# Performance work log

Measured on AMD Instinct MI355X. Metric: run time of the kernel, lower is better.

Reference implementation:

```python
import jax, jax.numpy as jnp
import numpy as np

N, E, IN_DIM, HID, LAYERS = 300000, 600000, 64, 128, 2
BN_EPS = 1e-5

def setup_inputs() -> dict:
    key = jax.random.key(0)
    ks = jax.random.split(key, 8)
    scale_in = 1.0 / np.sqrt(IN_DIM)
    scale_h = 1.0 / np.sqrt(HID)
    return {
        "node_init": jax.random.normal(ks[0], (N, IN_DIM), dtype=jnp.float32),
        "edge_index": jax.random.randint(ks[1], (2, E), 0, N, dtype=jnp.int64),
        "edge_len": jax.random.uniform(ks[2], (E,), dtype=jnp.float32),
        "W_in": jax.random.normal(ks[3], (IN_DIM, HID), dtype=jnp.float32) * scale_in,
        "b_in": jnp.zeros((HID,), dtype=jnp.float32),
        "att_k": jax.random.normal(ks[4], (HID,), dtype=jnp.float32),
        "Wl": jax.random.normal(ks[5], (LAYERS, HID, HID), dtype=jnp.float32) * scale_h,
        "bl": jnp.zeros((LAYERS, HID), dtype=jnp.float32),
        "gamma": jnp.ones((LAYERS, HID), dtype=jnp.float32),
        "beta": jnp.zeros((LAYERS, HID), dtype=jnp.float32),
    }

def reference(node_init, edge_index, edge_len, W_in, b_in, att_k, Wl, bl, gamma, beta):
    src, dst = edge_index[0], edge_index[1]
    inv_len = 1.0 / (1.0 + edge_len)                     # [E]
    inv_sqrt_h = 1.0 / jnp.sqrt(jnp.asarray(HID, node_init.dtype))
    h = node_init @ W_in + b_in                          # [N,H]
    n = h.shape[0]
    for l in range(LAYERS):
        h_src = h[src]                                   # [E,H] gather
        key = (h_src @ att_k) * inv_sqrt_h               # [E]
        w = jnp.exp(key) * inv_len                       # [E]
        agg = jax.ops.segment_sum(w[:, None] * h_src, dst, num_segments=n)  # [N,H]
        h = h + jax.nn.relu(agg) @ Wl[l] + bl[l]
        mean = jnp.mean(h, axis=0)
        var = jnp.mean((h - mean) ** 2, axis=0)          # biased var (BatchNorm training)
        h = (h - mean) * jax.lax.rsqrt(var + BN_EPS) * gamma[l] + beta[l]
    return h
```

## Files before the change

kernel.cpp:

```cpp
#include <hip/hip_runtime.h>
#include <hip/hip_bf16.h>

#define N_NODES 300000
#define N_EDGES 600000
#define IN_DIMC 64
#define HIDC    128
#define NLAYERS 2
#define BN_EPS  1e-5f
#define INV_SQRT_H 0.08838834764831845f
#define NB_SCAN ((N_NODES + 255) / 256)
#define NTILES  (N_NODES / 16)

typedef __bf16 bf16x8 __attribute__((ext_vector_type(8)));
typedef float floatx4 __attribute__((ext_vector_type(4)));

__device__ int   g_row_ptr[N_NODES + 1];
__device__ int   g_cursor[N_NODES];
__device__ __align__(8) int2 g_edge[N_EDGES];
__device__ __align__(8) int2 g_ew[N_EDGES];
__device__ int   g_bsum[NB_SCAN];
__device__ float g_ekey[N_NODES];
__device__ __align__(16) __hip_bfloat16 g_Win_hi[128 * 64];
__device__ __align__(16) __hip_bfloat16 g_Win_lo[128 * 64];
__device__ __align__(16) __hip_bfloat16 g_Wl_hi[NLAYERS * 128 * 128];
__device__ __align__(16) __hip_bfloat16 g_Wl_lo[NLAYERS * 128 * 128];
__device__ float g_stats[NLAYERS * 2 * HIDC];
__device__ __align__(16) float g_bn_sc[NLAYERS * HIDC];
__device__ __align__(16) float g_bn_sh[NLAYERS * HIDC];

__device__ inline void split2(float x, __hip_bfloat16& hi, __hip_bfloat16& lo) {
    hi = __float2bfloat16(x);
    lo = __float2bfloat16(x - __bfloat162float(hi));
}

__global__ void zero_kernel() {
    int i = blockIdx.x * 256 + threadIdx.x;
    if (i < N_NODES) g_cursor[i] = 0;
    if (i < NLAYERS * 2 * HIDC) g_stats[i] = 0.f;
}

__global__ void prep_w_kernel(const float* __restrict__ W_in,
                              const float* __restrict__ Wl)
{
    int id = blockIdx.x * 256 + threadIdx.x;
    if (id < 128 * 64) {
        int n = id >> 6, k = id & 63;
        split2(W_in[k * 128 + n], g_Win_hi[id], g_Win_lo[id]);
    }
    if (id < NLAYERS * 128 * 128) {
        int l = id >> 14, r = id & 16383;
        int n = r >> 7, k = r & 127;
        split2(Wl[l * 16384 + k * 128 + n], g_Wl_hi[id], g_Wl_lo[id]);
    }
}

__global__ void hist_kernel(const int* __restrict__ dst)
{
    int e = blockIdx.x * 256 + threadIdx.x;
    if (e < N_EDGES) atomicAdd(&g_cursor[dst[e]], 1);
}

__global__ void scan1_kernel()
{
    __shared__ int tmp[256];
    int t = threadIdx.x;
    int i = blockIdx.x * 256 + t;
    tmp[t] = (i < N_NODES) ? g_cursor[i] : 0;
    __syncthreads();
    for (int d = 128; d > 0; d >>= 1) {
        if (t < d) tmp[t] += tmp[t + d];
        __syncthreads();
    }
    if (t == 0) g_bsum[blockIdx.x] = tmp[0];
}

__global__ void scan2_kernel()
{
    __shared__ int tmp[256];
    __shared__ int carry;
    int t = threadIdx.x;
    if (t == 0) { carry = 0; g_row_ptr[N_NODES] = N_EDGES; }
    __syncthreads();
    for (int base = 0; base < NB_SCAN; base += 256) {
        int i = base + t;
        int v = (i < NB_SCAN) ? g_bsum[i] : 0;
        tmp[t] = v;
        __syncthreads();
        for (int d = 1; d < 256; d <<= 1) {
            int x = (t >= d) ? tmp[t - d] : 0;
            __syncthreads();
            tmp[t] += x;
            __syncthreads();
        }
        int c = carry;
        if (i < NB_SCAN) g_bsum[i] = c + tmp[t] - v;
        __syncthreads();
        if (t == 0) carry = c + tmp[255];
        __syncthreads();
    }
}

__global__ void scan3_kernel()
{
    __shared__ int tmp[256];
    int t = threadIdx.x;
    int i = blockIdx.x * 256 + t;
    int v = (i < N_NODES) ? g_cursor[i] : 0;
    tmp[t] = v;
    __syncthreads();
    for (int d = 1; d < 256; d <<= 1) {
        int x = (t >= d) ? tmp[t - d] : 0;
        __syncthreads();
        tmp[t] += x;
        __syncthreads();
    }
    int r = g_bsum[blockIdx.x] + tmp[t] - v;
    if (i < N_NODES) { g_row_ptr[i] = r; g_cursor[i] = r; }
}

__global__ void scatter_kernel(const int* __restrict__ src, const int* __restrict__ dst,
                               const float* __restrict__ elen)
{
    int e = blockIdx.x * 256 + threadIdx.x;
    if (e >= N_EDGES) return;
    int d = dst[e];
    int pos = atomicAdd(&g_cursor[d], 1);
    int2 ed;
    ed.x = src[e];
    ed.y = __float_as_int(1.0f / (1.0f + elen[e]));
    g_edge[pos] = ed;
}

__global__ __launch_bounds__(256) void wt_kernel()
{
    int e = blockIdx.x * 256 + threadIdx.x;
    if (e >= N_EDGES) return;
    int2 ed = g_edge[e];
    int2 ew;
    ew.x = ed.x;
    ew.y = __float_as_int(g_ekey[ed.x] * __int_as_float(ed.y));
    g_ew[e] = ew;
}

__global__ __launch_bounds__(256) void edge_csr_kernel(
    const float* __restrict__ h, __hip_bfloat16* __restrict__ agg_hi,
    __hip_bfloat16* __restrict__ agg_lo, int prev)
{
    int lane = threadIdx.x & 63;
    int n = blockIdx.x * 4 + (threadIdx.x >> 6);
    if (n >= N_NODES) return;
    int beg = g_row_ptr[n], end = g_row_ptr[n + 1];
    float a0 = 0.f, a1 = 0.f, sw = 0.f;
    const float2* h2 = (const float2*)h;
    for (int j = beg; j < end; j += 4) {
        int2 e0 = g_ew[j];
        int2 e1 = (j + 1 < end) ? g_ew[j + 1] : make_int2(e0.x, 0);
        int2 e2 = (j + 2 < end) ? g_ew[j + 2] : make_int2(e0.x, 0);
        int2 e3 = (j + 3 < end) ? g_ew[j + 3] : make_int2(e0.x, 0);
        float w0 = __int_as_float(e0.y);
        float w1 = __int_as_float(e1.y);
        float w2 = __int_as_float(e2.y);
        float w3 = __int_as_float(e3.y);
        float2 x0 = h2[(size_t)e0.x * 64 + lane];
        float2 x1 = h2[(size_t)e1.x * 64 + lane];
        float2 x2 = h2[(size_t)e2.x * 64 + lane];
        float2 x3 = h2[(size_t)e3.x * 64 + lane];
        a0 += w0 * x0.x + w1 * x1.x + w2 * x2.x + w3 * x3.x;
        a1 += w0 * x0.y + w1 * x1.y + w2 * x2.y + w3 * x3.y;
        sw += w0 + w1 + w2 + w3;
    }
    float2 sc = make_float2(1.f, 1.f), sh = make_float2(0.f, 0.f);
    if (prev >= 0) {
        sc = ((const float2*)(g_bn_sc + prev * HIDC))[lane];
        sh = ((const float2*)(g_bn_sh + prev * HIDC))[lane];
    }
    float o0 = fmaxf(sc.x * a0 + sh.x * sw, 0.f);
    float o1 = fmaxf(sc.y * a1 + sh.y * sw, 0.f);
    union { __hip_bfloat16 e[2]; unsigned u; } ph, pl;
    split2(o0, ph.e[0], pl.e[0]);
    split2(o1, ph.e[1], pl.e[1]);
    ((unsigned*)agg_hi)[(size_t)n * 64 + lane] = ph.u;
    ((unsigned*)agg_lo)[(size_t)n * 64 + lane] = pl.u;
}

__global__ __launch_bounds__(256) void proj_mfma_kernel(
    const float* __restrict__ X, const float* __restrict__ b,
    const float* __restrict__ att_k, float* __restrict__ h)
{
    __shared__ __align__(16) __hip_bfloat16 Ah[64 * 72];
    __shared__ __align__(16) __hip_bfloat16 Al[64 * 72];
    __shared__ __align__(16) __hip_bfloat16 Bh[128 * 72];
    __shared__ __align__(16) __hip_bfloat16 Bl[128 * 72];
    int t = threadIdx.x;
    int nbase = blockIdx.x * 64;

    for (int i = t; i < 1024; i += 256) {
        int row = i >> 3, c8 = i & 7;
        *(float4*)((char*)Bh + row * 144 + c8 * 16) =
            *(const float4*)((const char*)g_Win_hi + row * 128 + c8 * 16);
        *(float4*)((char*)Bl + row * 144 + c8 * 16) =
            *(const float4*)((const char*)g_Win_lo + row * 128 + c8 * 16);
    }
    for (int i = t; i < 1024; i += 256) {
        int row = i >> 4, c4 = i & 15;
        int n = nbase + row;
        float4 v = make_float4(0.f, 0.f, 0.f, 0.f);
        if (n < N_NODES) v = *(const float4*)(X + (size_t)n * IN_DIMC + c4 * 4);
        union { __hip_bfloat16 e[4]; uint2 u; } ph, pl;
        split2(v.x, ph.e[0], pl.e[0]); split2(v.y, ph.e[1], pl.e[1]);
        split2(v.z, ph.e[2], pl.e[2]); split2(v.w, ph.e[3], pl.e[3]);
        *(uint2*)((char*)Ah + row * 144 + c4 * 8) = ph.u;
        *(uint2*)((char*)Al + row * 144 + c4 * 8) = pl.u;
    }
    __syncthreads();

    int lane = t & 63, w = t >> 6;
    int m16 = lane & 15, quad = lane >> 4;
    floatx4 acc[8];
#pragma unroll
    for (int i = 0; i < 8; ++i) acc[i] = floatx4{0.f, 0.f, 0.f, 0.f};

#pragma unroll
    for (int kk = 0; kk < 64; kk += 32) {
        bf16x8 ah = *(const bf16x8*)((const char*)Ah + (w * 16 + m16) * 144 + (kk + quad * 8) * 2);
        bf16x8 al = *(const bf16x8*)((const char*)Al + (w * 16 + m16) * 144 + (kk + quad * 8) * 2);
#pragma unroll
        for (int nt = 0; nt < 8; ++nt) {
            bf16x8 bh = *(const bf16x8*)((const char*)Bh + (nt * 16 + m16) * 144 + (kk + quad * 8) * 2);
            bf16x8 bl = *(const bf16x8*)((const char*)Bl + (nt * 16 + m16) * 144 + (kk + quad * 8) * 2);
            acc[nt] = __builtin_amdgcn_mfma_f32_16x16x32_bf16(ah, bh, acc[nt], 0, 0, 0);
            acc[nt] = __builtin_amdgcn_mfma_f32_16x16x32_bf16(al, bh, acc[nt], 0, 0, 0);
            acc[nt] = __builtin_amdgcn_mfma_f32_16x16x32_bf16(ah, bl, acc[nt], 0, 0, 0);
        }
    }
    float dotr[4] = {0.f, 0.f, 0.f, 0.f};
#pragma unroll
    for (int nt = 0; nt < 8; ++nt) {
        int ch = nt * 16 + m16;
        float bias = b[ch];
        float ak = att_k[ch];
#pragma unroll
        for (int r = 0; r < 4; ++r) {
            int n = nbase + w * 16 + quad * 4 + r;
            float o = acc[nt][r] + bias;
            if (n < N_NODES) h[(size_t)n * HIDC + ch] = o;
            dotr[r] += ak * o;
        }
    }
#pragma unroll
    for (int r = 0; r < 4; ++r) {
        float p = dotr[r];
        p += __shfl_xor(p, 1); p += __shfl_xor(p, 2);
        p += __shfl_xor(p, 4); p += __shfl_xor(p, 8);
        int n = nbase + w * 16 + quad * 4 + r;
        if (m16 == 0 && n < N_NODES) g_ekey[n] = __expf(p * INV_SQRT_H);
    }
}

__global__ __launch_bounds__(256) void key_kernel(const float* __restrict__ h,
                                                  const float* __restrict__ att_k,
                                                  int prev)
{
    int t = threadIdx.x;
    int lane = t & 63;
    int half = lane >> 5, sub = lane & 31;
    int n = (blockIdx.x * 4 + (t >> 6)) * 2 + half;
    if (n >= N_NODES) return;
    float4 x = ((const float4*)h)[(size_t)n * 32 + sub];
    float4 sc = ((const float4*)(g_bn_sc + prev * HIDC))[sub];
    float4 sh = ((const float4*)(g_bn_sh + prev * HIDC))[sub];
    float4 ak = ((const float4*)att_k)[sub];
    float p = (sc.x * x.x + sh.x) * ak.x + (sc.y * x.y + sh.y) * ak.y +
              (sc.z * x.z + sh.z) * ak.z + (sc.w * x.w + sh.w) * ak.w;
    p += __shfl_xor(p, 1);  p += __shfl_xor(p, 2);
    p += __shfl_xor(p, 4);  p += __shfl_xor(p, 8);
    p += __shfl_xor(p, 16);
    if (sub == 0) g_ekey[n] = __expf(p * INV_SQRT_H);
}

__global__ __launch_bounds__(256) void layer_gemm_kernel(
    float* __restrict__ h, const __hip_bfloat16* __restrict__ agg_hi,
    const __hip_bfloat16* __restrict__ agg_lo,
    const float* __restrict__ b, int layer, int prev)
{
    __shared__ __align__(16) __hip_bfloat16 Bh[128 * 136];
    __shared__ __align__(16) __hip_bfloat16 Bl[128 * 136];
    __shared__ float red[256];
    int t = threadIdx.x;
    const __hip_bfloat16* Wh = g_Wl_hi + layer * 16384;
    const __hip_bfloat16* Wlo = g_Wl_lo + layer * 16384;
    red[t] = 0.f;

    for (int i = t; i < 2048; i += 256) {
        int row = i >> 4, c8 = i & 15;
        *(float4*)((char*)Bh + row * 272 + c8 * 16) =
            *(const float4*)((const char*)Wh + row * 256 + c8 * 16);
        *(float4*)((char*)Bl + row * 272 + c8 * 16) =
            *(const float4*)((const char*)Wlo + row * 256 + c8 * 16);
    }
    __syncthreads();

    const int lane = t & 63, w = t >> 6;
    const int m16 = lane & 15, quad = lane >> 4;
    const int wid = blockIdx.x * 4 + w;
    const int nwaves = gridDim.x * 4;

    float bias[8], scp[8], shp[8];
#pragma unroll
    for (int nt = 0; nt < 8; ++nt) {
        int ch = nt * 16 + m16;
        bias[nt] = b[ch];
        scp[nt] = (prev >= 0) ? g_bn_sc[prev * HIDC + ch] : 1.f;
        shp[nt] = (prev >= 0) ? g_bn_sh[prev * HIDC + ch] : 0.f;
    }
    float sreg[8], qreg[8];
#pragma unroll
    for (int nt = 0; nt < 8; ++nt) { sreg[nt] = 0.f; qreg[nt] = 0.f; }

    for (int tile = wid; tile < NTILES; tile += nwaves) {
        const __hip_bfloat16* ahp = agg_hi + (size_t)(tile * 16 + m16) * HIDC + quad * 8;
        const __hip_bfloat16* alp = agg_lo + (size_t)(tile * 16 + m16) * HIDC + quad * 8;
        floatx4 acc[8];
#pragma unroll
        for (int i = 0; i < 8; ++i) acc[i] = floatx4{0.f, 0.f, 0.f, 0.f};

#pragma unroll
        for (int kk = 0; kk < 4; ++kk) {
            bf16x8 ah = *(const bf16x8*)(ahp + kk * 32);
            bf16x8 al = *(const bf16x8*)(alp + kk * 32);
#pragma unroll
            for (int nt = 0; nt < 8; ++nt) {
                bf16x8 bh = *(const bf16x8*)((const char*)Bh + (nt * 16 + m16) * 272 + (kk * 32 + quad * 8) * 2);
                bf16x8 bl = *(const bf16x8*)((const char*)Bl + (nt * 16 + m16) * 272 + (kk * 32 + quad * 8) * 2);
                acc[nt] = __builtin_amdgcn_mfma_f32_16x16x32_bf16(ah, bh, acc[nt], 0, 0, 0);
                acc[nt] = __builtin_amdgcn_mfma_f32_16x16x32_bf16(al, bh, acc[nt], 0, 0, 0);
                acc[nt] = __builtin_amdgcn_mfma_f32_16x16x32_bf16(ah, bl, acc[nt], 0, 0, 0);
            }
        }
        int node0 = tile * 16 + quad * 4;
#pragma unroll
        for (int nt = 0; nt < 8; ++nt) {
            int ch = nt * 16 + m16;
#pragma unroll
            for (int r = 0; r < 4; ++r) {
                float* hp = h + (size_t)(node0 + r) * HIDC + ch;
                float o = scp[nt] * (*hp) + shp[nt] + acc[nt][r] + bias[nt];
                *hp = o;
                sreg[nt] += o;
                qreg[nt] += o * o;
            }
        }
    }

#pragma unroll
    for (int nt = 0; nt < 8; ++nt) {
        float s = sreg[nt], q = qreg[nt];
        s += __shfl_xor(s, 16); s += __shfl_xor(s, 32);
        q += __shfl_xor(q, 16); q += __shfl_xor(q, 32);
        if (quad == 0) {
            atomicAdd(&red[nt * 16 + m16], s);
            atomicAdd(&red[HIDC + nt * 16 + m16], q);
        }
    }
    __syncthreads();
    atomicAdd(&g_stats[layer * 2 * HIDC + t], red[t]);
}

__global__ void bn_prep_kernel(const float* __restrict__ gamma,
                               const float* __restrict__ beta, int layer)
{
    int c = threadIdx.x;
    if (c >= HIDC) return;
    const float invN = 1.0f / (float)N_NODES;
    float mean = g_stats[layer * 2 * HIDC + c] * invN;
    float var = g_stats[layer * 2 * HIDC + HIDC + c] * invN - mean * mean;
    float s = gamma[layer * HIDC + c] * rsqrtf(var + BN_EPS);
    g_bn_sc[layer * HIDC + c] = s;
    g_bn_sh[layer * HIDC + c] = beta[layer * HIDC + c] - mean * s;
}

__global__ __launch_bounds__(256) void bn_apply_kernel(float* __restrict__ h, int layer)
{
    size_t idx = (size_t)blockIdx.x * 256 + threadIdx.x;
    if (idx >= (size_t)N_NODES * (HIDC / 4)) return;
    int cg = (int)(idx & 31);
    float4 sc = ((const float4*)(g_bn_sc + layer * HIDC))[cg];
    float4 sh = ((const float4*)(g_bn_sh + layer * HIDC))[cg];
    float4 v = ((float4*)h)[idx];
    v.x = sc.x * v.x + sh.x;
    v.y = sc.y * v.y + sh.y;
    v.z = sc.z * v.z + sh.z;
    v.w = sc.w * v.w + sh.w;
    ((float4*)h)[idx] = v;
}

extern "C" void kernel_launch(void* const* d_in, const int* in_sizes, int n_in,
                              void* d_out, int out_size, void* d_ws, size_t ws_size,
                              hipStream_t stream) {
    (void)in_sizes; (void)n_in; (void)out_size; (void)ws_size;
    const float* node_init = (const float*)d_in[0];
    const int*   eidx      = (const int*)d_in[1];
    const float* elen      = (const float*)d_in[2];
    const float* W_in      = (const float*)d_in[3];
    const float* b_in      = (const float*)d_in[4];
    const float* att_k     = (const float*)d_in[5];
    const float* Wl        = (const float*)d_in[6];
    const float* bl        = (const float*)d_in[7];
    const float* gamma     = (const float*)d_in[8];
    const float* beta      = (const float*)d_in[9];

    float* h = (float*)d_out;
    __hip_bfloat16* agg_hi = (__hip_bfloat16*)d_ws;
    __hip_bfloat16* agg_lo = agg_hi + (size_t)N_NODES * HIDC;

    const int* src = eidx;
    const int* dst = eidx + N_EDGES;

    zero_kernel<<<NB_SCAN, 256, 0, stream>>>();
    hist_kernel<<<(N_EDGES + 255) / 256, 256, 0, stream>>>(dst);
    scan1_kernel<<<NB_SCAN, 256, 0, stream>>>();
    scan2_kernel<<<1, 256, 0, stream>>>();
    scan3_kernel<<<NB_SCAN, 256, 0, stream>>>();
    scatter_kernel<<<(N_EDGES + 255) / 256, 256, 0, stream>>>(src, dst, elen);
    prep_w_kernel<<<(NLAYERS * 128 * 128 + 255) / 256, 256, 0, stream>>>(W_in, Wl);

    proj_mfma_kernel<<<(N_NODES + 63) / 64, 256, 0, stream>>>(node_init, b_in, att_k, h);

    for (int l = 0; l < NLAYERS; ++l) {
        if (l > 0)
            key_kernel<<<(N_NODES / 2 + 3) / 4, 256, 0, stream>>>(h, att_k, l - 1);
        wt_kernel<<<(N_EDGES + 255) / 256, 256, 0, stream>>>();
        edge_csr_kernel<<<(N_NODES + 3) / 4, 256, 0, stream>>>(h, agg_hi, agg_lo, l - 1);
        layer_gemm_kernel<<<512, 256, 0, stream>>>(h, agg_hi, agg_lo, bl + (size_t)l * HIDC, l, l - 1);
        bn_prep_kernel<<<1, 128, 0, stream>>>(gamma, beta, l);
    }
    bn_apply_kernel<<<(N_NODES * (HIDC / 4) + 255) / 256, 256, 0, stream>>>(h, NLAYERS - 1);
}
```

Baseline: 890.0 us.

## Fuse first-layer edge weights into scatter and use half-wave per node aggregation

Moves the projection kernel ahead of the CSR scatter so the scatter can compute layer-0 edge weights directly from the freshly written node keys, removing the first wt_kernel launch and its pass over the edge list. The edge aggregation kernel now assigns 32 lanes per node with float4 loads, two nodes per wavefront, and 2-edge unrolling instead of 4. This cuts the number of gather instructions per edge. In exchange it reduces per-thread memory-level parallelism and adds more divergence between nodes of different degree within a wave.

```diff
diff --git a/kernel.cpp b/kernel.cpp
--- a/kernel.cpp
+++ b/kernel.cpp
@@ -124,11 +124,17 @@
     int e = blockIdx.x * 256 + threadIdx.x;
     if (e >= N_EDGES) return;
     int d = dst[e];
+    int s = src[e];
     int pos = atomicAdd(&g_cursor[d], 1);
+    float il = 1.0f / (1.0f + elen[e]);
     int2 ed;
-    ed.x = src[e];
-    ed.y = __float_as_int(1.0f / (1.0f + elen[e]));
+    ed.x = s;
+    ed.y = __float_as_int(il);
     g_edge[pos] = ed;
+    int2 ew;
+    ew.x = s;
+    ew.y = __float_as_int(g_ekey[s] * il);
+    g_ew[pos] = ew;
 }
 
 __global__ __launch_bounds__(256) void wt_kernel()
@@ -146,41 +152,44 @@
     const float* __restrict__ h, __hip_bfloat16* __restrict__ agg_hi,
     __hip_bfloat16* __restrict__ agg_lo, int prev)
 {
-    int lane = threadIdx.x & 63;
-    int n = blockIdx.x * 4 + (threadIdx.x >> 6);
+    int t = threadIdx.x;
+    int lane = t & 63;
+    int half = lane >> 5, sub = lane & 31;
+    int n = (blockIdx.x * 4 + (t >> 6)) * 2 + half;
     if (n >= N_NODES) return;
     int beg = g_row_ptr[n], end = g_row_ptr[n + 1];
-    float a0 = 0.f, a1 = 0.f, sw = 0.f;
-    const float2* h2 = (const float2*)h;
-    for (int j = beg; j < end; j += 4) {
+    float ax = 0.f, ay = 0.f, az = 0.f, aw = 0.f, sw = 0.f;
+    const float4* h4 = (const float4*)h;
+    for (int j = beg; j < end; j += 2) {
         int2 e0 = g_ew[j];
         int2 e1 = (j + 1 < end) ? g_ew[j + 1] : make_int2(e0.x, 0);
-        int2 e2 = (j + 2 < end) ? g_ew[j + 2] : make_int2(e0.x, 0);
-        int2 e3 = (j + 3 < end) ? g_ew[j + 3] : make_int2(e0.x, 0);
         float w0 = __int_as_float(e0.y);
         float w1 = __int_as_float(e1.y);
-        float w2 = __int_as_float(e2.y);
-        float w3 = __int_as_float(e3.y);
-        float2 x0 = h2[(size_t)e0.x * 64 + lane];
-        float2 x1 = h2[(size_t)e1.x * 64 + lane];
-        float2 x2 = h2[(size_t)e2.x * 64 + lane];
-        float2 x3 = h2[(size_t)e3.x * 64 + lane];
-        a0 += w0 * x0.x + w1 * x1.x + w2 * x2.x + w3 * x3.x;
-        a1 += w0 * x0.y + w1 * x1.y + w2 * x2.y + w3 * x3.y;
-        sw += w0 + w1 + w2 + w3;
-    }
-    float2 sc = make_float2(1.f, 1.f), sh = make_float2(0.f, 0.f);
+        float4 x0 = h4[(size_t)e0.x * 32 + sub];
+        float4 x1 = h4[(size_t)e1.x * 32 + sub];
+        ax += w0 * x0.x + w1 * x1.x;
+        ay += w0 * x0.y + w1 * x1.y;
+        az += w0 * x0.z + w1 * x1.z;
+        aw += w0 * x0.w + w1 * x1.w;
+        sw += w0 + w1;
+    }
+    float4 sc = make_float4(1.f, 1.f, 1.f, 1.f);
+    float4 sh = make_float4(0.f, 0.f, 0.f, 0.f);
     if (prev >= 0) {
-        sc = ((const float2*)(g_bn_sc + prev * HIDC))[lane];
-        sh = ((const float2*)(g_bn_sh + prev * HIDC))[lane];
-    }
-    float o0 = fmaxf(sc.x * a0 + sh.x * sw, 0.f);
-    float o1 = fmaxf(sc.y * a1 + sh.y * sw, 0.f);
-    union { __hip_bfloat16 e[2]; unsigned u; } ph, pl;
+        sc = ((const float4*)(g_bn_sc + prev * HIDC))[sub];
+        sh = ((const float4*)(g_bn_sh + prev * HIDC))[sub];
+    }
+    float o0 = fmaxf(sc.x * ax + sh.x * sw, 0.f);
+    float o1 = fmaxf(sc.y * ay + sh.y * sw, 0.f);
+    float o2 = fmaxf(sc.z * az + sh.z * sw, 0.f);
+    float o3 = fmaxf(sc.w * aw + sh.w * sw, 0.f);
+    union { __hip_bfloat16 e[4]; uint2 u; } ph, pl;
     split2(o0, ph.e[0], pl.e[0]);
     split2(o1, ph.e[1], pl.e[1]);
-    ((unsigned*)agg_hi)[(size_t)n * 64 + lane] = ph.u;
-    ((unsigned*)agg_lo)[(size_t)n * 64 + lane] = pl.u;
+    split2(o2, ph.e[2], pl.e[2]);
+    split2(o3, ph.e[3], pl.e[3]);
+    ((uint2*)agg_hi)[(size_t)n * 32 + sub] = ph.u;
+    ((uint2*)agg_lo)[(size_t)n * 32 + sub] = pl.u;
 }
 
 __global__ __launch_bounds__(256) void proj_mfma_kernel(
@@ -421,16 +430,17 @@
     scan1_kernel<<<NB_SCAN, 256, 0, stream>>>();
     scan2_kernel<<<1, 256, 0, stream>>>();
     scan3_kernel<<<NB_SCAN, 256, 0, stream>>>();
+    prep_w_kernel<<<(NLAYERS * 128 * 128 + 255) / 256, 256, 0, stream>>>(W_in, Wl);
+
+    proj_mfma_kernel<<<(N_NODES + 63) / 64, 256, 0, stream>>>(node_init, b_in, att_k, h);
     scatter_kernel<<<(N_EDGES + 255) / 256, 256, 0, stream>>>(src, dst, elen);
-    prep_w_kernel<<<(NLAYERS * 128 * 128 + 255) / 256, 256, 0, stream>>>(W_in, Wl);
-
-    proj_mfma_kernel<<<(N_NODES + 63) / 64, 256, 0, stream>>>(node_init, b_in, att_k, h);
 
     for (int l = 0; l < NLAYERS; ++l) {
-        if (l > 0)
+        if (l > 0) {
             key_kernel<<<(N_NODES / 2 + 3) / 4, 256, 0, stream>>>(h, att_k, l - 1);
-        wt_kernel<<<(N_EDGES + 255) / 256, 256, 0, stream>>>();
-        edge_csr_kernel<<<(N_NODES + 3) / 4, 256, 0, stream>>>(h, agg_hi, agg_lo, l - 1);
+            wt_kernel<<<(N_EDGES + 255) / 256, 256, 0, stream>>>();
+        }
+        edge_csr_kernel<<<(N_NODES + 7) / 8, 256, 0, stream>>>(h, agg_hi, agg_lo, l - 1);
         layer_gemm_kernel<<<512, 256, 0, stream>>>(h, agg_hi, agg_lo, bl + (size_t)l * HIDC, l, l - 1);
         bn_prep_kernel<<<1, 128, 0, stream>>>(gamma, beta, l);
     }
```

Result: faster. 832.1 us (-6.5%).
